# Optimization experiments

Hardware: AMD Instinct MI355X
Metric: run time of the kernel (lower is better)

Reference implementation:

```python
import jax, jax.numpy as jnp
import numpy as np

D_MODEL = 1024
N_HEADS = 16
HEAD_DIM = D_MODEL // N_HEADS
SOFTMAX_SCALE = 1.0 / np.sqrt(HEAD_DIM).astype(np.float32)


def setup_inputs() -> dict:
    key = jax.random.key(0)
    k1, k2, k3, k4, k5 = jax.random.split(key, 5)
    B, S = 2, 2048
    bound_qkv = 1.0 / np.sqrt(D_MODEL)
    x = jax.random.normal(k1, (B, S, D_MODEL), dtype=jnp.float32)
    # torch nn.Linear stores weight as [out_features, in_features]
    Wqkv_w = jax.random.uniform(k2, (3 * D_MODEL, D_MODEL), jnp.float32, -bound_qkv, bound_qkv)
    Wqkv_b = jax.random.uniform(k3, (3 * D_MODEL,), jnp.float32, -bound_qkv, bound_qkv)
    Wout_w = jax.random.uniform(k4, (D_MODEL, D_MODEL), jnp.float32, -bound_qkv, bound_qkv)
    Wout_b = jax.random.uniform(k5, (D_MODEL,), jnp.float32, -bound_qkv, bound_qkv)
    return {"x": x, "Wqkv_w": Wqkv_w, "Wqkv_b": Wqkv_b, "Wout_w": Wout_w, "Wout_b": Wout_b}


def reference(x, Wqkv_w, Wqkv_b, Wout_w, Wout_b):
    B, S, D = x.shape
    # fused QKV projection
    qkv = jnp.einsum('bsd,ed->bse', x, Wqkv_w) + Wqkv_b  # [B, S, 3D]
    q, k, v = jnp.split(qkv, 3, axis=2)
    # b s (h d) -> b h s d
    q = q.reshape(B, S, N_HEADS, HEAD_DIM).transpose(0, 2, 1, 3)
    k = k.reshape(B, S, N_HEADS, HEAD_DIM).transpose(0, 2, 1, 3)
    v = v.reshape(B, S, N_HEADS, HEAD_DIM).transpose(0, 2, 1, 3)
    attn = jnp.einsum('bhsd,bhtd->bhst', q, k) * SOFTMAX_SCALE
    attn = jax.nn.softmax(attn, axis=-1)
    ctx = jnp.einsum('bhst,bhtd->bhsd', attn, v)
    ctx = ctx.transpose(0, 2, 1, 3).reshape(B, S, D)
    out = jnp.einsum('bsd,ed->bse', ctx, Wout_w) + Wout_b
    return out
```

## Files before the change

### kernel.cpp

```cpp
#include <hip/hip_runtime.h>
#include <hip/hip_bf16.h>

typedef __attribute__((ext_vector_type(8))) __bf16 bfrag;
typedef __attribute__((ext_vector_type(4))) float f32x4;
typedef __attribute__((ext_vector_type(16))) float f32x16;
typedef __attribute__((ext_vector_type(8))) unsigned short u16x8;
typedef __attribute__((ext_vector_type(4))) unsigned short u16x4;
typedef __attribute__((ext_vector_type(4))) unsigned int u32x4;

#define SEQ 2048
#define NH 16
#define HD 64
#define DMODEL 1024
#define MTOT 4096
#define QSCALE 0.18033688011112042f

static __device__ __forceinline__ unsigned short f2bf(float f) {
  unsigned int u = __builtin_bit_cast(unsigned int, f);
  u += 0x7FFFu + ((u >> 16) & 1u);
  return (unsigned short)(u >> 16);
}

static __device__ __forceinline__ unsigned cvt_pk_bf16(float lo, float hi) {
  unsigned r;
  asm("v_cvt_pk_bf16_f32 %0, %1, %2" : "=v"(r) : "v"(lo), "v"(hi));
  return r;
}

static __device__ __forceinline__ float rsum16(const f32x16 v) {
  float a0 = v[0] + v[1], a1 = v[2] + v[3], a2 = v[4] + v[5], a3 = v[6] + v[7];
  float a4 = v[8] + v[9], a5 = v[10] + v[11], a6 = v[12] + v[13], a7 = v[14] + v[15];
  float b0 = a0 + a1, b1 = a2 + a3, b2 = a4 + a5, b3 = a6 + a7;
  return (b0 + b1) + (b2 + b3);
}

#define XG 524288
#define WQG 393216
#define WOG 131072
__global__ __launch_bounds__(256) void cvt_all_kernel(const float* __restrict__ x,
                                                      const float* __restrict__ wq,
                                                      const float* __restrict__ wo,
                                                      unsigned short* __restrict__ out) {
  int i = blockIdx.x * 256 + threadIdx.x;
  if (i >= XG + WQG + WOG) return;
  const float4* p;
  if (i < XG) p = reinterpret_cast<const float4*>(x) + (size_t)i * 2;
  else if (i < XG + WQG) p = reinterpret_cast<const float4*>(wq) + (size_t)(i - XG) * 2;
  else p = reinterpret_cast<const float4*>(wo) + (size_t)(i - XG - WQG) * 2;
  float4 a = p[0], b = p[1];
  u16x8 o;
  o[0] = f2bf(a.x); o[1] = f2bf(a.y); o[2] = f2bf(a.z); o[3] = f2bf(a.w);
  o[4] = f2bf(b.x); o[5] = f2bf(b.y); o[6] = f2bf(b.z); o[7] = f2bf(b.w);
  *(reinterpret_cast<u16x8*>(out) + i) = o;
}

#define GLDS(gp, lp)                                                       \
  __builtin_amdgcn_global_load_lds(                                        \
      (const __attribute__((address_space(1))) void*)(gp),                 \
      (__attribute__((address_space(3))) void*)(lp), 16, 0, 0)

template <int EPI>
__global__ __launch_bounds__(256) void gemm_bt_kernel(
    const unsigned short* __restrict__ A, const unsigned short* __restrict__ B,
    const float* __restrict__ bias, unsigned short* __restrict__ q_out,
    unsigned short* __restrict__ k_out, unsigned short* __restrict__ v_out,
    float* __restrict__ f_out, int M, int N, int K) {
  __shared__ __align__(16) unsigned short As[3][4096];
  __shared__ __align__(16) unsigned short Bs[3][4096];
  const int t = threadIdx.x;
  const int l = t & 63, w = t >> 6;
  const int m0 = blockIdx.y * 128, n0 = blockIdx.x * 128;
  const int wrow = (w >> 1) * 64, wcol = (w & 1) * 64;
  const int lrow = l & 15, lk = (l >> 4) * 8;
  const int srow = t >> 2;
  const int scol = ((t & 3) ^ (srow & 3)) * 8;
  f32x4 acc[4][4] = {};

#define GSTAGE(buf, K0)                                                     \
  do {                                                                      \
    GLDS(A + (size_t)(m0 + srow) * K + (K0) + scol, &As[buf][0] + t * 8);   \
    GLDS(A + (size_t)(m0 + srow + 64) * K + (K0) + scol,                    \
         &As[buf][0] + 2048 + t * 8);                                       \
    GLDS(B + (size_t)(n0 + srow) * K + (K0) + scol, &Bs[buf][0] + t * 8);   \
    GLDS(B + (size_t)(n0 + srow + 64) * K + (K0) + scol,                    \
         &Bs[buf][0] + 2048 + t * 8);                                       \
  } while (0)

  const int nsteps = K >> 5;
  GSTAGE(0, 0);
  GSTAGE(1, 32);
#pragma unroll 1
  for (int ks = 0; ks < nsteps; ++ks) {
    if (ks < nsteps - 1)
      asm volatile("s_waitcnt vmcnt(4)" ::: "memory");
    else
      asm volatile("s_waitcnt vmcnt(0)" ::: "memory");
    __builtin_amdgcn_s_barrier();
    __builtin_amdgcn_sched_barrier(0);
    if (ks + 2 < nsteps) GSTAGE((ks + 2) % 3, (ks + 2) * 32);
    const unsigned short* Ac = &As[ks % 3][0];
    const unsigned short* Bc = &Bs[ks % 3][0];
    bfrag af[4], bf[4];
#pragma unroll
    for (int mt = 0; mt < 4; ++mt) {
      int row = wrow + mt * 16 + lrow;
      af[mt] = *(const bfrag*)&Ac[row * 32 + (lk ^ ((row & 3) << 3))];
    }
#pragma unroll
    for (int nt = 0; nt < 4; ++nt) {
      int row = wcol + nt * 16 + lrow;
      bf[nt] = *(const bfrag*)&Bc[row * 32 + (lk ^ ((row & 3) << 3))];
    }
#pragma unroll
    for (int mt = 0; mt < 4; ++mt)
#pragma unroll
      for (int nt = 0; nt < 4; ++nt)
        acc[mt][nt] =
            __builtin_amdgcn_mfma_f32_16x16x32_bf16(af[mt], bf[nt], acc[mt][nt], 0, 0, 0);
  }
#undef GSTAGE
#pragma unroll
  for (int nt = 0; nt < 4; ++nt) {
    int gn = n0 + wcol + nt * 16 + lrow;
    float bv = bias[gn];
    if constexpr (EPI == 0) {
      int sel = gn >> 10;
      int e = gn & 1023;
      int h = e >> 6, d = e & 63;
#pragma unroll
      for (int mt = 0; mt < 4; ++mt) {
#pragma unroll
        for (int r = 0; r < 4; ++r) {
          int gm = m0 + wrow + mt * 16 + (l >> 4) * 4 + r;
          int b = gm >> 11, s = gm & 2047;
          float fv = acc[mt][nt][r] + bv;
          if (sel == 0)
            q_out[((size_t)(b * NH + h) * SEQ + s) * HD + d] = f2bf(fv * QSCALE);
          else if (sel == 1)
            k_out[((size_t)(b * NH + h) * SEQ + s) * HD + d] = f2bf(fv);
          else
            v_out[((size_t)(b * NH + h) * HD + d) * SEQ + s] = f2bf(fv);
        }
      }
    } else {
#pragma unroll
      for (int mt = 0; mt < 4; ++mt) {
#pragma unroll
        for (int r = 0; r < 4; ++r) {
          int gm = m0 + wrow + mt * 16 + (l >> 4) * 4 + r;
          f_out[(size_t)gm * N + gn] = acc[mt][nt][r] + bv;
        }
      }
    }
  }
}

__global__ __launch_bounds__(256, 2)
void attn_kernel(const unsigned short* __restrict__ Q,
                 const unsigned short* __restrict__ Km,
                 const unsigned short* __restrict__ Vt,
                 unsigned short* __restrict__ Ctx) {
  __shared__ __align__(16) unsigned short Ks[2][128 * 64];
  __shared__ __align__(16) unsigned short Vs[2][64 * 128];
  const int t = threadIdx.x;
  const int l = t & 63, w = t >> 6;
  const int q31 = l & 31, h = l >> 5;
  const int lid = blockIdx.y * gridDim.x + blockIdx.x;
  const int bh = (lid & 7) * 4 + ((lid >> 3) >> 4);
  const int q0 = ((lid >> 3) & 15) * 128 + w * 32;
  const unsigned short* qb = Q + (size_t)bh * SEQ * HD;
  const unsigned short* kb = Km + (size_t)bh * SEQ * HD;
  const unsigned short* vb = Vt + (size_t)bh * HD * SEQ;

  bfrag qf[4];
#pragma unroll
  for (int c = 0; c < 4; ++c)
    qf[c] = *(const bfrag*)&qb[(size_t)(q0 + q31) * HD + c * 16 + h * 8];

  f32x16 acc0 = {}, acc1 = {};
  float llocal = 0.f;

  const int skr = t >> 3;
  const int sks = ((t & 7) ^ (skr & 7)) * 8;
  const int svr = t >> 4;
  const int svs = ((t & 15) ^ svr) * 8;

#define STAGE(buf, T)                                                          \
  do {                                                                         \
    const int kv0_ = (T) * 128;                                                \
    _Pragma("unroll") for (int j = 0; j < 4; ++j)                              \
        GLDS(kb + (size_t)(kv0_ + 32 * j + skr) * HD + sks,                    \
             &Ks[buf][0] + j * 2048 + t * 8);                                  \
    _Pragma("unroll") for (int j = 0; j < 4; ++j)                              \
        GLDS(vb + (size_t)(16 * j + svr) * SEQ + kv0_ + svs,                   \
             &Vs[buf][0] + j * 2048 + t * 8);                                  \
  } while (0)

  STAGE(0, 0);
  __syncthreads();

  const int sw7 = q31 & 7, sw15 = q31 & 15;

#pragma unroll 1
  for (int t2 = 0; t2 < 16; ++t2) {
    if (t2 < 15) STAGE((t2 + 1) & 1, t2 + 1);
    const unsigned short* Kc = &Ks[t2 & 1][0];
    const unsigned short* Vc = &Vs[t2 & 1][0];
#pragma unroll
    for (int st = 0; st < 4; ++st) {
      bfrag kf[4];
#pragma unroll
      for (int c = 0; c < 4; ++c)
        kf[c] = *(const bfrag*)&Kc[(st * 32 + q31) * 64 + (((2 * c + h) ^ sw7) * 8)];
      f32x16 s = {};
      __builtin_amdgcn_s_setprio(1);
#pragma unroll
      for (int c = 0; c < 4; ++c)
        s = __builtin_amdgcn_mfma_f32_32x32x16_bf16(kf[c], qf[c], s, 0, 0, 0);
      __builtin_amdgcn_s_setprio(0);
#pragma unroll
      for (int r = 0; r < 16; ++r) s[r] = __builtin_amdgcn_exp2f(s[r]);
      llocal += rsum16(s);
#pragma unroll
      for (int u = 0; u < 2; ++u) {
        const int win = st * 2 + u;
        const int bse = u * 8;
        unsigned pk0 = cvt_pk_bf16(s[bse + 0], s[bse + 1]);
        unsigned pk1 = cvt_pk_bf16(s[bse + 2], s[bse + 3]);
        unsigned pk2 = cvt_pk_bf16(s[bse + 4], s[bse + 5]);
        unsigned pk3 = cvt_pk_bf16(s[bse + 6], s[bse + 7]);
        auto w02 = __builtin_amdgcn_permlane32_swap(pk0, pk2, false, false);
        auto w13 = __builtin_amdgcn_permlane32_swap(pk1, pk3, false, false);
        u32x4 bw = {(unsigned)w02[0], (unsigned)w13[0], (unsigned)w02[1], (unsigned)w13[1]};
        bfrag pb = __builtin_bit_cast(bfrag, bw);
        const int vchunk = ((win * 2 + h) ^ sw15) * 8;
        bfrag vf0 = *(const bfrag*)&Vc[q31 * 128 + vchunk];
        bfrag vf1 = *(const bfrag*)&Vc[(32 + q31) * 128 + vchunk];
        __builtin_amdgcn_s_setprio(1);
        acc0 = __builtin_amdgcn_mfma_f32_32x32x16_bf16(vf0, pb, acc0, 0, 0, 0);
        acc1 = __builtin_amdgcn_mfma_f32_32x32x16_bf16(vf1, pb, acc1, 0, 0, 0);
        __builtin_amdgcn_s_setprio(0);
      }
    }
    __syncthreads();
  }
#undef STAGE

  const int b = bh >> 4, head = bh & 15;
  float lsum = llocal + __shfl_xor(llocal, 32);
  const float inv = __builtin_amdgcn_rcpf(lsum);
  unsigned short* cp = Ctx + ((size_t)(b * SEQ + (q0 + q31)) * NH + head) * HD;
#pragma unroll
  for (int dt = 0; dt < 2; ++dt) {
    const f32x16 av = dt ? acc1 : acc0;
#pragma unroll
    for (int rq = 0; rq < 4; ++rq) {
      u16x4 o;
#pragma unroll
      for (int rr = 0; rr < 4; ++rr) o[rr] = f2bf(av[rq * 4 + rr] * inv);
      *(u16x4*)&cp[dt * 32 + rq * 8 + h * 4] = o;
    }
  }
}

extern "C" void kernel_launch(void* const* d_in, const int* in_sizes, int n_in,
                              void* d_out, int out_size, void* d_ws, size_t ws_size,
                              hipStream_t stream) {
  const float* x = (const float*)d_in[0];
  const float* wqkv = (const float*)d_in[1];
  const float* bqkv = (const float*)d_in[2];
  const float* wout = (const float*)d_in[3];
  const float* bout = (const float*)d_in[4];
  float* out = (float*)d_out;

  unsigned short* xb = (unsigned short*)d_ws;
  unsigned short* wqkvb = xb + (size_t)MTOT * DMODEL;
  unsigned short* woutb = wqkvb + (size_t)3 * DMODEL * DMODEL;
  unsigned short* qb = woutb + (size_t)DMODEL * DMODEL;
  unsigned short* kb = qb + (size_t)32 * SEQ * HD;
  unsigned short* vtb = kb + (size_t)32 * SEQ * HD;
  unsigned short* ctxb = vtb + (size_t)32 * SEQ * HD;

  cvt_all_kernel<<<(XG + WQG + WOG + 255) / 256, 256, 0, stream>>>(x, wqkv, wout, xb);
  gemm_bt_kernel<0><<<dim3(3 * DMODEL / 128, MTOT / 128), 256, 0, stream>>>(
      xb, wqkvb, bqkv, qb, kb, vtb, nullptr, MTOT, 3 * DMODEL, DMODEL);
  attn_kernel<<<dim3(SEQ / 128, 32), 256, 0, stream>>>(qb, kb, vtb, ctxb);
  gemm_bt_kernel<1><<<dim3(DMODEL / 128, MTOT / 128), 256, 0, stream>>>(
      ctxb, woutb, bout, nullptr, nullptr, nullptr, out, MTOT, DMODEL, DMODEL);
}
```

Measured before the change: 121.2 us.

## Software-pipeline QK^T with softmax/PV and stagger sub-tile order per wave

Restructures the attention inner loop so the QK^T MFMAs for the next 32-key sub-tile are issued before the exp/convert/PV work of the current one. This lets matrix-core work overlap the transcendental and permute work. Each wave also starts at a different sub-tile (w & 3), which spreads LDS bank access across waves. The next tile's async global-to-LDS stage is now issued after the first QK block rather than at the top of the iteration. The price is higher register pressure from holding two score tiles and two K fragment sets.

```diff
diff --git a/kernel.cpp b/kernel.cpp
--- a/kernel.cpp
+++ b/kernel.cpp
@@ -200,51 +200,75 @@
   __syncthreads();
 
   const int sw7 = q31 & 7, sw15 = q31 & 15;
+  const int st0 = w & 3;
+
+#define LOADK(kfv, stx)                                                        \
+  _Pragma("unroll") for (int c = 0; c < 4; ++c)                                \
+      kfv[c] = *(const bfrag*)&Kc[((stx) * 32 + q31) * 64 +                    \
+                                  (((2 * c + h) ^ sw7) * 8)]
+
+#define QK4(dst, kfv)                                                          \
+  do {                                                                         \
+    dst = (f32x16){};                                                          \
+    __builtin_amdgcn_s_setprio(1);                                             \
+    _Pragma("unroll") for (int c = 0; c < 4; ++c)                              \
+        dst = __builtin_amdgcn_mfma_f32_32x32x16_bf16(kfv[c], qf[c], dst, 0, 0, 0); \
+    __builtin_amdgcn_s_setprio(0);                                             \
+  } while (0)
+
+#define SOFTPV(stx, SV)                                                        \
+  do {                                                                         \
+    _Pragma("unroll") for (int r = 0; r < 16; ++r)                             \
+        SV[r] = __builtin_amdgcn_exp2f(SV[r]);                                 \
+    llocal += rsum16(SV);                                                      \
+    _Pragma("unroll") for (int u = 0; u < 2; ++u) {                            \
+      const int win = (stx) * 2 + u;                                           \
+      const int bse = u * 8;                                                   \
+      unsigned pk0 = cvt_pk_bf16(SV[bse + 0], SV[bse + 1]);                    \
+      unsigned pk1 = cvt_pk_bf16(SV[bse + 2], SV[bse + 3]);                    \
+      unsigned pk2 = cvt_pk_bf16(SV[bse + 4], SV[bse + 5]);                    \
+      unsigned pk3 = cvt_pk_bf16(SV[bse + 6], SV[bse + 7]);                    \
+      auto w02 = __builtin_amdgcn_permlane32_swap(pk0, pk2, false, false);     \
+      auto w13 = __builtin_amdgcn_permlane32_swap(pk1, pk3, false, false);     \
+      u32x4 bw = {(unsigned)w02[0], (unsigned)w13[0], (unsigned)w02[1],        \
+                  (unsigned)w13[1]};                                           \
+      bfrag pb = __builtin_bit_cast(bfrag, bw);                                \
+      const int vchunk = ((win * 2 + h) ^ sw15) * 8;                           \
+      bfrag vf0 = *(const bfrag*)&Vc[q31 * 128 + vchunk];                      \
+      bfrag vf1 = *(const bfrag*)&Vc[(32 + q31) * 128 + vchunk];               \
+      __builtin_amdgcn_s_setprio(1);                                           \
+      acc0 = __builtin_amdgcn_mfma_f32_32x32x16_bf16(vf0, pb, acc0, 0, 0, 0);  \
+      acc1 = __builtin_amdgcn_mfma_f32_32x32x16_bf16(vf1, pb, acc1, 0, 0, 0);  \
+      __builtin_amdgcn_s_setprio(0);                                           \
+    }                                                                          \
+  } while (0)
 
 #pragma unroll 1
   for (int t2 = 0; t2 < 16; ++t2) {
-    if (t2 < 15) STAGE((t2 + 1) & 1, t2 + 1);
     const unsigned short* Kc = &Ks[t2 & 1][0];
     const unsigned short* Vc = &Vs[t2 & 1][0];
-#pragma unroll
-    for (int st = 0; st < 4; ++st) {
-      bfrag kf[4];
-#pragma unroll
-      for (int c = 0; c < 4; ++c)
-        kf[c] = *(const bfrag*)&Kc[(st * 32 + q31) * 64 + (((2 * c + h) ^ sw7) * 8)];
-      f32x16 s = {};
-      __builtin_amdgcn_s_setprio(1);
-#pragma unroll
-      for (int c = 0; c < 4; ++c)
-        s = __builtin_amdgcn_mfma_f32_32x32x16_bf16(kf[c], qf[c], s, 0, 0, 0);
-      __builtin_amdgcn_s_setprio(0);
-#pragma unroll
-      for (int r = 0; r < 16; ++r) s[r] = __builtin_amdgcn_exp2f(s[r]);
-      llocal += rsum16(s);
-#pragma unroll
-      for (int u = 0; u < 2; ++u) {
-        const int win = st * 2 + u;
-        const int bse = u * 8;
-        unsigned pk0 = cvt_pk_bf16(s[bse + 0], s[bse + 1]);
-        unsigned pk1 = cvt_pk_bf16(s[bse + 2], s[bse + 3]);
-        unsigned pk2 = cvt_pk_bf16(s[bse + 4], s[bse + 5]);
-        unsigned pk3 = cvt_pk_bf16(s[bse + 6], s[bse + 7]);
-        auto w02 = __builtin_amdgcn_permlane32_swap(pk0, pk2, false, false);
-        auto w13 = __builtin_amdgcn_permlane32_swap(pk1, pk3, false, false);
-        u32x4 bw = {(unsigned)w02[0], (unsigned)w13[0], (unsigned)w02[1], (unsigned)w13[1]};
-        bfrag pb = __builtin_bit_cast(bfrag, bw);
-        const int vchunk = ((win * 2 + h) ^ sw15) * 8;
-        bfrag vf0 = *(const bfrag*)&Vc[q31 * 128 + vchunk];
-        bfrag vf1 = *(const bfrag*)&Vc[(32 + q31) * 128 + vchunk];
-        __builtin_amdgcn_s_setprio(1);
-        acc0 = __builtin_amdgcn_mfma_f32_32x32x16_bf16(vf0, pb, acc0, 0, 0, 0);
-        acc1 = __builtin_amdgcn_mfma_f32_32x32x16_bf16(vf1, pb, acc1, 0, 0, 0);
-        __builtin_amdgcn_s_setprio(0);
+    bfrag kfa[4], kfb[4];
+    f32x16 scur, snxt;
+    LOADK(kfa, st0);
+    QK4(scur, kfa);
+    if (t2 < 15) STAGE((t2 + 1) & 1, t2 + 1);
+#pragma unroll
+    for (int j = 0; j < 4; ++j) {
+      if (j < 3) {
+        const int stn = (st0 + j + 1) & 3;
+        LOADK(kfb, stn);
+        QK4(snxt, kfb);
       }
+      const int stc = (st0 + j) & 3;
+      SOFTPV(stc, scur);
+      scur = snxt;
     }
     __syncthreads();
   }
 #undef STAGE
+#undef LOADK
+#undef QK4
+#undef SOFTPV
 
   const int b = bh >> 4, head = bh & 15;
   float lsum = llocal + __shfl_xor(llocal, 32);
```

After: 120.2 us. Within noise of the previous version (-0.8%).

## Split attention KV range in two halves with a separate combine kernel

Applied to the files above, without the earlier changes.

Attention work is split along the key/value axis into two halves. Each block processes 1024 keys in 64-key tiles, which halves shared memory and raises occupancy to 4 blocks per CU. The grid grows from 512 to 1024 blocks. Each half writes unnormalized bf16 partial context plus row sums into reused workspace (xb and wqkvb buffers), and a new reduce kernel adds the partials and normalizes. This relies on the softmax having no max subtraction, so partials can simply be summed. In exchange it adds an extra launch, extra memory traffic, and bf16 rounding of the partials before they are combined.

```diff
diff --git a/kernel.cpp b/kernel.cpp
--- a/kernel.cpp
+++ b/kernel.cpp
@@ -19,6 +19,11 @@
   unsigned int u = __builtin_bit_cast(unsigned int, f);
   u += 0x7FFFu + ((u >> 16) & 1u);
   return (unsigned short)(u >> 16);
+}
+
+static __device__ __forceinline__ float bf2f(unsigned short s) {
+  unsigned int u = (unsigned int)s << 16;
+  return __builtin_bit_cast(float, u);
 }
 
 static __device__ __forceinline__ unsigned cvt_pk_bf16(float lo, float hi) {
@@ -155,19 +160,23 @@
   }
 }
 
-__global__ __launch_bounds__(256, 2)
+__global__ __launch_bounds__(256, 4)
 void attn_kernel(const unsigned short* __restrict__ Q,
                  const unsigned short* __restrict__ Km,
                  const unsigned short* __restrict__ Vt,
-                 unsigned short* __restrict__ Ctx) {
-  __shared__ __align__(16) unsigned short Ks[2][128 * 64];
-  __shared__ __align__(16) unsigned short Vs[2][64 * 128];
+                 unsigned short* __restrict__ pA, unsigned short* __restrict__ pB,
+                 float* __restrict__ lsA, float* __restrict__ lsB) {
+  __shared__ __align__(16) unsigned short Ks[2][64 * 64];
+  __shared__ __align__(16) unsigned short Vs[2][64 * 64];
   const int t = threadIdx.x;
   const int l = t & 63, w = t >> 6;
   const int q31 = l & 31, h = l >> 5;
   const int lid = blockIdx.y * gridDim.x + blockIdx.x;
-  const int bh = (lid & 7) * 4 + ((lid >> 3) >> 4);
-  const int q0 = ((lid >> 3) & 15) * 128 + w * 32;
+  const int bh = (lid & 7) * 4 + ((lid >> 3) >> 5);
+  const int sub = (lid >> 3) & 31;
+  const int qc = sub >> 1, kvh = sub & 1;
+  const int q0 = qc * 128 + w * 32;
+  const int kvbase = kvh << 10;
   const unsigned short* qb = Q + (size_t)bh * SEQ * HD;
   const unsigned short* kb = Km + (size_t)bh * SEQ * HD;
   const unsigned short* vb = Vt + (size_t)bh * HD * SEQ;
@@ -180,67 +189,66 @@
   f32x16 acc0 = {}, acc1 = {};
   float llocal = 0.f;
 
-  const int skr = t >> 3;
-  const int sks = ((t & 7) ^ (skr & 7)) * 8;
-  const int svr = t >> 4;
-  const int svs = ((t & 15) ^ svr) * 8;
+  const int srow = t >> 3;
+  const int ssw = ((t & 7) ^ (srow & 7)) * 8;
 
 #define STAGE(buf, T)                                                          \
   do {                                                                         \
-    const int kv0_ = (T) * 128;                                                \
-    _Pragma("unroll") for (int j = 0; j < 4; ++j)                              \
-        GLDS(kb + (size_t)(kv0_ + 32 * j + skr) * HD + sks,                    \
-             &Ks[buf][0] + j * 2048 + t * 8);                                  \
-    _Pragma("unroll") for (int j = 0; j < 4; ++j)                              \
-        GLDS(vb + (size_t)(16 * j + svr) * SEQ + kv0_ + svs,                   \
-             &Vs[buf][0] + j * 2048 + t * 8);                                  \
+    const int kv0_ = kvbase + (T) * 64;                                        \
+    GLDS(kb + (size_t)(kv0_ + srow) * HD + ssw, &Ks[buf][0] + t * 8);          \
+    GLDS(kb + (size_t)(kv0_ + 32 + srow) * HD + ssw,                           \
+         &Ks[buf][0] + 2048 + t * 8);                                          \
+    GLDS(vb + (size_t)srow * SEQ + kv0_ + ssw, &Vs[buf][0] + t * 8);           \
+    GLDS(vb + (size_t)(32 + srow) * SEQ + kv0_ + ssw,                          \
+         &Vs[buf][0] + 2048 + t * 8);                                          \
   } while (0)
 
   STAGE(0, 0);
   __syncthreads();
 
-  const int sw7 = q31 & 7, sw15 = q31 & 15;
+  const int swz = q31 & 7;
 
 #pragma unroll 1
   for (int t2 = 0; t2 < 16; ++t2) {
     if (t2 < 15) STAGE((t2 + 1) & 1, t2 + 1);
     const unsigned short* Kc = &Ks[t2 & 1][0];
     const unsigned short* Vc = &Vs[t2 & 1][0];
-#pragma unroll
-    for (int st = 0; st < 4; ++st) {
-      bfrag kf[4];
-#pragma unroll
-      for (int c = 0; c < 4; ++c)
-        kf[c] = *(const bfrag*)&Kc[(st * 32 + q31) * 64 + (((2 * c + h) ^ sw7) * 8)];
-      f32x16 s = {};
+    bfrag kf[8], vf[8];
+#pragma unroll
+    for (int i = 0; i < 8; ++i) {
+      const int off = ((i >> 2) * 32 + q31) * 64 + ((((i & 3) * 2 + h) ^ swz) * 8);
+      kf[i] = *(const bfrag*)&Kc[off];
+      vf[i] = *(const bfrag*)&Vc[off];
+    }
+    f32x16 s0 = {}, s1 = {};
+    __builtin_amdgcn_s_setprio(1);
+#pragma unroll
+    for (int c = 0; c < 4; ++c) {
+      s0 = __builtin_amdgcn_mfma_f32_32x32x16_bf16(kf[c], qf[c], s0, 0, 0, 0);
+      s1 = __builtin_amdgcn_mfma_f32_32x32x16_bf16(kf[4 + c], qf[c], s1, 0, 0, 0);
+    }
+    __builtin_amdgcn_s_setprio(0);
+#pragma unroll
+    for (int r = 0; r < 16; ++r) s0[r] = __builtin_amdgcn_exp2f(s0[r]);
+#pragma unroll
+    for (int r = 0; r < 16; ++r) s1[r] = __builtin_amdgcn_exp2f(s1[r]);
+    llocal += rsum16(s0) + rsum16(s1);
+#pragma unroll
+    for (int cg = 0; cg < 4; ++cg) {
+      const f32x16 sv = (cg < 2) ? s0 : s1;
+      const int bse = (cg & 1) * 8;
+      unsigned pk0 = cvt_pk_bf16(sv[bse + 0], sv[bse + 1]);
+      unsigned pk1 = cvt_pk_bf16(sv[bse + 2], sv[bse + 3]);
+      unsigned pk2 = cvt_pk_bf16(sv[bse + 4], sv[bse + 5]);
+      unsigned pk3 = cvt_pk_bf16(sv[bse + 6], sv[bse + 7]);
+      auto w02 = __builtin_amdgcn_permlane32_swap(pk0, pk2, false, false);
+      auto w13 = __builtin_amdgcn_permlane32_swap(pk1, pk3, false, false);
+      u32x4 bw = {(unsigned)w02[0], (unsigned)w13[0], (unsigned)w02[1], (unsigned)w13[1]};
+      bfrag pb = __builtin_bit_cast(bfrag, bw);
       __builtin_amdgcn_s_setprio(1);
-#pragma unroll
-      for (int c = 0; c < 4; ++c)
-        s = __builtin_amdgcn_mfma_f32_32x32x16_bf16(kf[c], qf[c], s, 0, 0, 0);
+      acc0 = __builtin_amdgcn_mfma_f32_32x32x16_bf16(vf[cg], pb, acc0, 0, 0, 0);
+      acc1 = __builtin_amdgcn_mfma_f32_32x32x16_bf16(vf[4 + cg], pb, acc1, 0, 0, 0);
       __builtin_amdgcn_s_setprio(0);
-#pragma unroll
-      for (int r = 0; r < 16; ++r) s[r] = __builtin_amdgcn_exp2f(s[r]);
-      llocal += rsum16(s);
-#pragma unroll
-      for (int u = 0; u < 2; ++u) {
-        const int win = st * 2 + u;
-        const int bse = u * 8;
-        unsigned pk0 = cvt_pk_bf16(s[bse + 0], s[bse + 1]);
-        unsigned pk1 = cvt_pk_bf16(s[bse + 2], s[bse + 3]);
-        unsigned pk2 = cvt_pk_bf16(s[bse + 4], s[bse + 5]);
-        unsigned pk3 = cvt_pk_bf16(s[bse + 6], s[bse + 7]);
-        auto w02 = __builtin_amdgcn_permlane32_swap(pk0, pk2, false, false);
-        auto w13 = __builtin_amdgcn_permlane32_swap(pk1, pk3, false, false);
-        u32x4 bw = {(unsigned)w02[0], (unsigned)w13[0], (unsigned)w02[1], (unsigned)w13[1]};
-        bfrag pb = __builtin_bit_cast(bfrag, bw);
-        const int vchunk = ((win * 2 + h) ^ sw15) * 8;
-        bfrag vf0 = *(const bfrag*)&Vc[q31 * 128 + vchunk];
-        bfrag vf1 = *(const bfrag*)&Vc[(32 + q31) * 128 + vchunk];
-        __builtin_amdgcn_s_setprio(1);
-        acc0 = __builtin_amdgcn_mfma_f32_32x32x16_bf16(vf0, pb, acc0, 0, 0, 0);
-        acc1 = __builtin_amdgcn_mfma_f32_32x32x16_bf16(vf1, pb, acc1, 0, 0, 0);
-        __builtin_amdgcn_s_setprio(0);
-      }
     }
     __syncthreads();
   }
@@ -248,8 +256,10 @@
 
   const int b = bh >> 4, head = bh & 15;
   float lsum = llocal + __shfl_xor(llocal, 32);
-  const float inv = __builtin_amdgcn_rcpf(lsum);
-  unsigned short* cp = Ctx + ((size_t)(b * SEQ + (q0 + q31)) * NH + head) * HD;
+  unsigned short* pX = kvh ? pB : pA;
+  float* lsX = kvh ? lsB : lsA;
+  if (h == 0) lsX[(size_t)bh * SEQ + q0 + q31] = lsum;
+  unsigned short* cp = pX + ((size_t)(b * SEQ + (q0 + q31)) * NH + head) * HD;
 #pragma unroll
   for (int dt = 0; dt < 2; ++dt) {
     const f32x16 av = dt ? acc1 : acc0;
@@ -257,10 +267,28 @@
     for (int rq = 0; rq < 4; ++rq) {
       u16x4 o;
 #pragma unroll
-      for (int rr = 0; rr < 4; ++rr) o[rr] = f2bf(av[rq * 4 + rr] * inv);
+      for (int rr = 0; rr < 4; ++rr) o[rr] = f2bf(av[rq * 4 + rr]);
       *(u16x4*)&cp[dt * 32 + rq * 8 + h * 4] = o;
     }
   }
+}
+
+__global__ __launch_bounds__(256) void reduce_kernel(unsigned short* __restrict__ pA,
+                                                     const unsigned short* __restrict__ pB,
+                                                     const float* __restrict__ lsA,
+                                                     const float* __restrict__ lsB) {
+  int i = blockIdx.x * 256 + threadIdx.x;
+  if (i >= 524288) return;
+  const int m = i >> 7, e8 = i & 127;
+  const int b = m >> 11, s = m & 2047, h = e8 >> 3;
+  const size_t lidx = ((size_t)(b * NH + h)) * SEQ + s;
+  const float inv = __builtin_amdgcn_rcpf(lsA[lidx] + lsB[lidx]);
+  u16x8 a = *(const u16x8*)(pA + (size_t)i * 8);
+  u16x8 bb = *(const u16x8*)(pB + (size_t)i * 8);
+  u16x8 o;
+#pragma unroll
+  for (int j = 0; j < 8; ++j) o[j] = f2bf((bf2f(a[j]) + bf2f(bb[j])) * inv);
+  *(u16x8*)(pA + (size_t)i * 8) = o;
 }
 
 extern "C" void kernel_launch(void* const* d_in, const int* in_sizes, int n_in,
@@ -281,10 +309,15 @@
   unsigned short* vtb = kb + (size_t)32 * SEQ * HD;
   unsigned short* ctxb = vtb + (size_t)32 * SEQ * HD;
 
+  unsigned short* pB = xb;
+  float* lsA = (float*)wqkvb;
+  float* lsB = lsA + (size_t)32 * SEQ;
+
   cvt_all_kernel<<<(XG + WQG + WOG + 255) / 256, 256, 0, stream>>>(x, wqkv, wout, xb);
   gemm_bt_kernel<0><<<dim3(3 * DMODEL / 128, MTOT / 128), 256, 0, stream>>>(
       xb, wqkvb, bqkv, qb, kb, vtb, nullptr, MTOT, 3 * DMODEL, DMODEL);
-  attn_kernel<<<dim3(SEQ / 128, 32), 256, 0, stream>>>(qb, kb, vtb, ctxb);
+  attn_kernel<<<dim3(32, 32), 256, 0, stream>>>(qb, kb, vtb, ctxb, pB, lsA, lsB);
+  reduce_kernel<<<2048, 256, 0, stream>>>(ctxb, pB, lsA, lsB);
   gemm_bt_kernel<1><<<dim3(DMODEL / 128, MTOT / 128), 256, 0, stream>>>(
       ctxb, woutb, bout, nullptr, nullptr, nullptr, out, MTOT, DMODEL, DMODEL);
 }
```

Result: slower. 202.8 us (+67.3%).
